# Performance work log

Hardware: AMD Instinct MI355X
Metric: run time of the kernel (lower is better)

## Reference

```python
import jax, jax.numpy as jnp
import numpy as np

N = 4
SEGMENTS = 16
IN_F = 256
OUT_F = 256
BATCH = 512


def chebyshev_lobatto(n):
    # Chebyshev-Lobatto interpolation nodes on [-1, 1]
    k = jnp.arange(n, dtype=jnp.float32)
    return -jnp.cos(jnp.pi * k / (n - 1))


def lagrange_basis(x, nodes):
    # x: [B, In]; returns basis values [B, In, n]
    n = nodes.shape[0]
    cols = []
    for j in range(n):  # n is a small static constant (4)
        terms = [(x - nodes[m]) / (nodes[j] - nodes[m]) for m in range(n) if m != j]
        cols.append(jnp.prod(jnp.stack(terms, axis=0), axis=0))
    return jnp.stack(cols, axis=-1)


def setup_inputs() -> dict:
    key = jax.random.key(0)
    k1, k2 = jax.random.split(key)
    x = jax.random.uniform(k1, (BATCH, IN_F), dtype=jnp.float32, minval=-1.0, maxval=1.0)
    w = jax.random.uniform(
        k2, (OUT_F, IN_F, (N - 1) * SEGMENTS + 1), dtype=jnp.float32, minval=-1.0, maxval=1.0
    )
    return {"x": x, "w": w, "n": N, "segments": SEGMENTS}


def reference(x, w, n, segments):
    nodes = chebyshev_lobatto(n)
    # segment id per element, clamped to [0, segments-1]
    id_min = jnp.clip(((x + 1.0) / 2.0 * segments).astype(jnp.int32), 0, segments - 1)
    id_max = id_min + 1
    wid_min = id_min * (n - 1)  # start of weight slice; slice length == n
    # segment boundaries in x-space: eta(i) = i/segments * 2 - 1
    x_min = id_min.astype(x.dtype) / segments * 2.0 - 1.0
    x_max = id_max.astype(x.dtype) / segments * 2.0 - 1.0
    # rescale x into [-1, 1] within its segment
    x_in = 2.0 * (x - x_min) / (x_max - x_min) - 1.0
    basis = lagrange_basis(x_in, nodes)  # [B, In, n]
    # gather per-element weight slice: w_g[b,i,j,o] = w[o, i, wid_min[b,i]+j]
    idx = wid_min[..., None] + jnp.arange(n)  # [B, In, n]
    w_t = jnp.transpose(w, (1, 2, 0))  # [In, K, Out]
    in_f = w.shape[1]
    w_g = w_t[jnp.arange(in_f)[None, :, None], idx]  # [B, In, n, Out]
    # interpolate and sum over in_features (matches einsum 'ijk,jkli->jl')
    return jnp.einsum("bin,bino->bo", basis, w_g)
```

## Files before the change

kernel.cpp:

```cpp
#include <hip/hip_runtime.h>


typedef _Float16 h2 __attribute__((ext_vector_type(2)));

#define INF     256
#define OUTF    256
#define WSTRIDE 49
#define OSTRIDE (INF * WSTRIDE)
#define PSLICE  (512 * 256)
#define WE_U2   (256 * 16 * 256)
#define BT_U4   (512 * 256)

#define GLOAD16(gptr, lptr)                                                         \
  __builtin_amdgcn_global_load_lds(                                                 \
      (const __attribute__((address_space(1))) unsigned int*)(gptr),                \
      (__attribute__((address_space(3))) unsigned int*)(lptr), 16, 0, 0)

__global__ __launch_bounds__(256)
void pp_prep(const float* __restrict__ x, const float* __restrict__ w,
             uint2* __restrict__ we, uint4* __restrict__ bt) {
    const int blk = blockIdx.x;
    if (blk < 256) {
        const int i = blk, o = threadIdx.x;
        const float* src = w + (size_t)o * OSTRIDE + i * WSTRIDE;
        float t[49];
        #pragma unroll
        for (int k = 0; k < 49; ++k) t[k] = src[k];
        #pragma unroll
        for (int s = 0; s < 16; ++s) {
            auto p0 = __builtin_amdgcn_cvt_pkrtz(t[3*s],   t[3*s+1]);
            auto p1 = __builtin_amdgcn_cvt_pkrtz(t[3*s+2], t[3*s+3]);
            uint2 v;
            v.x = __builtin_bit_cast(unsigned int, p0);
            v.y = __builtin_bit_cast(unsigned int, p1);
            we[((size_t)i * 16 + s) * 256 + o] = v;
        }
    } else {
        const int e = (blk - 256) * 1024 + threadIdx.x * 4;
        float4 xv = *(const float4*)(x + e);
        const float xs[4] = {xv.x, xv.y, xv.z, xv.w};
        #pragma unroll
        for (int q = 0; q < 4; ++q) {
            float xx = xs[q];
            int id = (int)((xx + 1.0f) * 8.0f);
            id = id < 0 ? 0 : (id > 15 ? 15 : id);
            float u = (xx - ((float)id * 0.125f - 1.0f)) * 16.0f - 1.0f;
            float a = u + 1.0f, b2 = u + 0.5f, cc = u - 0.5f, d = u - 1.0f;
            float c0 = b2 * cc * d  * (-2.0f / 3.0f);
            float c1 = a  * cc * d  * ( 4.0f / 3.0f);
            float c2 = a  * b2 * d  * (-4.0f / 3.0f);
            float c3 = a  * b2 * cc * ( 2.0f / 3.0f);
            auto pA = __builtin_amdgcn_cvt_pkrtz(c0, c1);
            auto pB = __builtin_amdgcn_cvt_pkrtz(c2, c3);
            uint4 v;
            v.x = __builtin_bit_cast(unsigned int, pA);
            v.y = __builtin_bit_cast(unsigned int, pB);
            v.z = (unsigned int)id;
            v.w = 0u;
            bt[e + q] = v;
        }
    }
}

__global__ __launch_bounds__(256, 2)
void pp_main(const uint2* __restrict__ we, const uint4* __restrict__ bt,
             float* __restrict__ part) {
    __shared__ uint2 wt[8192];

    const int tid  = threadIdx.x;
    const int wave = __builtin_amdgcn_readfirstlane(tid >> 6);
    const int lane = tid & 63;
    const int i_base = blockIdx.x * 8;
    const int o_base = blockIdx.y * 64;
    const int b0     = blockIdx.z * 128 + wave * 32;

    #pragma unroll
    for (int it = 0; it < 16; ++it) {
        const int u = it * 256 + tid;
        const int i = u >> 9, s = (u >> 5) & 15, g = u & 31;
        const unsigned int* gp = (const unsigned int*)we
            + ((((size_t)(i_base + i) * 16 + s) * 256) + o_base + g * 2) * 2;
        GLOAD16(gp, (unsigned int*)wt + (size_t)u * 4);
    }
    __syncthreads();

    const uint4* btp = bt + ((size_t)b0 * 256 + i_base);
    float* pout = part + (size_t)blockIdx.x * PSLICE + o_base + lane;

    for (int bb = 0; bb < 32; ++bb) {
        const uint4* be = btp + (size_t)bb * 256;
        float acc = 0.0f;
        #pragma unroll
        for (int i = 0; i < 8; ++i) {
            const uint4 B = be[i];
            const h2 cA = __builtin_bit_cast(h2, B.x);
            const h2 cB = __builtin_bit_cast(h2, B.y);
            const uint2 wv = wt[((i * 16 + (int)B.z) << 6) + lane];
            acc = __builtin_amdgcn_fdot2(__builtin_bit_cast(h2, wv.x), cA, acc, false);
            acc = __builtin_amdgcn_fdot2(__builtin_bit_cast(h2, wv.y), cB, acc, false);
        }
        pout[(size_t)(b0 + bb) * 256] = acc;
    }
}

__global__ __launch_bounds__(256)
void pp_reduce(const float* __restrict__ part, float* __restrict__ out) {
    const size_t off4 = (size_t)blockIdx.x * 256 + threadIdx.x;
    const float4* p4 = (const float4*)part;
    float4 s = make_float4(0.f, 0.f, 0.f, 0.f);
    #pragma unroll
    for (int k = 0; k < 32; ++k) {
        float4 v = p4[(size_t)k * (PSLICE / 4) + off4];
        s.x += v.x; s.y += v.y; s.z += v.z; s.w += v.w;
    }
    ((float4*)out)[off4] = s;
}

extern "C" void kernel_launch(void* const* d_in, const int* in_sizes, int n_in,
                              void* d_out, int out_size, void* d_ws, size_t ws_size,
                              hipStream_t stream) {
    const float* x = (const float*)d_in[0];
    const float* w = (const float*)d_in[1];
    float* out = (float*)d_out;
    uint2* we  = (uint2*)d_ws;
    uint4* bt  = (uint4*)((char*)d_ws + (size_t)WE_U2 * 8);
    float* part = (float*)((char*)d_ws + (size_t)WE_U2 * 8
                                       + (size_t)BT_U4 * 16);
    (void)ws_size; (void)n_in; (void)in_sizes; (void)out_size;

    pp_prep<<<dim3(384), 256, 0, stream>>>(x, w, we, bt);
    pp_main<<<dim3(32, 4, 4), 256, 0, stream>>>(we, bt, part);
    pp_reduce<<<dim3(128), 256, 0, stream>>>(part, out);
}
```

Measured before the change: 93.82 us.

## Recast segment-gather interpolation as one-hot dense GEMM on MFMA

The per-segment weight gather is replaced by a dense formulation. Basis coefficients are scattered into a one-hot, segment-expanded A matrix, and weights are laid out as a dense K=64-per-feature B matrix, both written in fp16. A tiled MFMA 16x16x32 GEMM with register-prefetched shared-memory staging computes the split-K partials. This trades a large increase in FLOPs and an extra workspace matrix (~16 MB written and read) for tensor-core throughput in place of scalar fdot2 with LDS gathers.

```diff
diff --git a/kernel.cpp b/kernel.cpp
--- a/kernel.cpp
+++ b/kernel.cpp
@@ -1,106 +1,154 @@
 #include <hip/hip_runtime.h>
 
 
-typedef _Float16 h2 __attribute__((ext_vector_type(2)));
+typedef _Float16 half8 __attribute__((ext_vector_type(8)));
+typedef float f32x4 __attribute__((ext_vector_type(4)));
 
-#define INF     256
-#define OUTF    256
-#define WSTRIDE 49
-#define OSTRIDE (INF * WSTRIDE)
+#define OSTRIDE 12544
 #define PSLICE  (512 * 256)
-#define WE_U2   (256 * 16 * 256)
-#define BT_U4   (512 * 256)
-
-#define GLOAD16(gptr, lptr)                                                         \
-  __builtin_amdgcn_global_load_lds(                                                 \
-      (const __attribute__((address_space(1))) unsigned int*)(gptr),                \
-      (__attribute__((address_space(3))) unsigned int*)(lptr), 16, 0, 0)
+#define WE_U4   (256 * 256 * 8)
+#define AT_U4   (256 * 512 * 8)
 
 __global__ __launch_bounds__(256)
 void pp_prep(const float* __restrict__ x, const float* __restrict__ w,
-             uint2* __restrict__ we, uint4* __restrict__ bt) {
+             uint4* __restrict__ we_t, uint4* __restrict__ A_t) {
+    __shared__ uint4 sm[256 * 9];
+    const int t = threadIdx.x;
     const int blk = blockIdx.x;
+
     if (blk < 256) {
-        const int i = blk, o = threadIdx.x;
-        const float* src = w + (size_t)o * OSTRIDE + i * WSTRIDE;
-        float t[49];
+        const int i = blk;
+        const float* src = w + (size_t)t * OSTRIDE + i * 49;
+        float v[49];
         #pragma unroll
-        for (int k = 0; k < 49; ++k) t[k] = src[k];
+        for (int k = 0; k < 49; ++k) v[k] = src[k];
         #pragma unroll
-        for (int s = 0; s < 16; ++s) {
-            auto p0 = __builtin_amdgcn_cvt_pkrtz(t[3*s],   t[3*s+1]);
-            auto p1 = __builtin_amdgcn_cvt_pkrtz(t[3*s+2], t[3*s+3]);
-            uint2 v;
-            v.x = __builtin_bit_cast(unsigned int, p0);
-            v.y = __builtin_bit_cast(unsigned int, p1);
-            we[((size_t)i * 16 + s) * 256 + o] = v;
+        for (int q = 0; q < 8; ++q) {
+            auto p0 = __builtin_amdgcn_cvt_pkrtz(v[6*q],   v[6*q+1]);
+            auto p1 = __builtin_amdgcn_cvt_pkrtz(v[6*q+2], v[6*q+3]);
+            auto p2 = __builtin_amdgcn_cvt_pkrtz(v[6*q+3], v[6*q+4]);
+            auto p3 = __builtin_amdgcn_cvt_pkrtz(v[6*q+5], v[6*q+6]);
+            uint4 u;
+            u.x = __builtin_bit_cast(unsigned int, p0);
+            u.y = __builtin_bit_cast(unsigned int, p1);
+            u.z = __builtin_bit_cast(unsigned int, p2);
+            u.w = __builtin_bit_cast(unsigned int, p3);
+            sm[t * 9 + q] = u;
+        }
+        __syncthreads();
+        #pragma unroll
+        for (int k = 0; k < 8; ++k) {
+            const int u = k * 256 + t;
+            we_t[(size_t)i * 2048 + u] = sm[(u >> 3) * 9 + (u & 7)];
         }
     } else {
-        const int e = (blk - 256) * 1024 + threadIdx.x * 4;
-        float4 xv = *(const float4*)(x + e);
-        const float xs[4] = {xv.x, xv.y, xv.z, xv.w};
+        const int z = blk - 256;
+        const int i = z >> 1;
+        const int b = (z & 1) * 256 + t;
+        const float xx = x[(size_t)b * 256 + i];
+        int id = (int)((xx + 1.0f) * 8.0f);
+        id = id < 0 ? 0 : (id > 15 ? 15 : id);
+        const float u = (xx - ((float)id * 0.125f - 1.0f)) * 16.0f - 1.0f;
+        const float a = u + 1.0f, b2 = u + 0.5f, cc = u - 0.5f, d = u - 1.0f;
+        const float c0 = b2 * cc * d  * (-2.0f / 3.0f);
+        const float c1 = a  * cc * d  * ( 4.0f / 3.0f);
+        const float c2 = a  * b2 * d  * (-4.0f / 3.0f);
+        const float c3 = a  * b2 * cc * ( 2.0f / 3.0f);
+        auto pA = __builtin_amdgcn_cvt_pkrtz(c0, c1);
+        auto pB = __builtin_amdgcn_cvt_pkrtz(c2, c3);
+        const uint4 z4 = make_uint4(0u, 0u, 0u, 0u);
         #pragma unroll
-        for (int q = 0; q < 4; ++q) {
-            float xx = xs[q];
-            int id = (int)((xx + 1.0f) * 8.0f);
-            id = id < 0 ? 0 : (id > 15 ? 15 : id);
-            float u = (xx - ((float)id * 0.125f - 1.0f)) * 16.0f - 1.0f;
-            float a = u + 1.0f, b2 = u + 0.5f, cc = u - 0.5f, d = u - 1.0f;
-            float c0 = b2 * cc * d  * (-2.0f / 3.0f);
-            float c1 = a  * cc * d  * ( 4.0f / 3.0f);
-            float c2 = a  * b2 * d  * (-4.0f / 3.0f);
-            float c3 = a  * b2 * cc * ( 2.0f / 3.0f);
-            auto pA = __builtin_amdgcn_cvt_pkrtz(c0, c1);
-            auto pB = __builtin_amdgcn_cvt_pkrtz(c2, c3);
-            uint4 v;
-            v.x = __builtin_bit_cast(unsigned int, pA);
-            v.y = __builtin_bit_cast(unsigned int, pB);
-            v.z = (unsigned int)id;
-            v.w = 0u;
-            bt[e + q] = v;
+        for (int q = 0; q < 8; ++q) sm[t * 9 + q] = z4;
+        unsigned int* smu = (unsigned int*)sm;
+        smu[t * 36 + 2 * id]     = __builtin_bit_cast(unsigned int, pA);
+        smu[t * 36 + 2 * id + 1] = __builtin_bit_cast(unsigned int, pB);
+        __syncthreads();
+        uint4* dst = A_t + ((size_t)i * 512 + (z & 1) * 256) * 8;
+        #pragma unroll
+        for (int k = 0; k < 8; ++k) {
+            const int uu = k * 256 + t;
+            dst[uu] = sm[(uu >> 3) * 9 + (uu & 7)];
         }
     }
 }
 
-__global__ __launch_bounds__(256, 2)
-void pp_main(const uint2* __restrict__ we, const uint4* __restrict__ bt,
+__global__ __launch_bounds__(256)
+void pp_gemm(const uint4* __restrict__ A_t, const uint4* __restrict__ we_t,
              float* __restrict__ part) {
-    __shared__ uint2 wt[8192];
+    __shared__ unsigned int smA[128 * 36];
+    __shared__ unsigned int smB[128 * 36];
 
-    const int tid  = threadIdx.x;
-    const int wave = __builtin_amdgcn_readfirstlane(tid >> 6);
-    const int lane = tid & 63;
-    const int i_base = blockIdx.x * 8;
-    const int o_base = blockIdx.y * 64;
-    const int b0     = blockIdx.z * 128 + wave * 32;
+    const int t = threadIdx.x;
+    const int wave = t >> 6, lane = t & 63;
+    const int quad = lane >> 4, l16 = lane & 15;
+    const int ks = blockIdx.x;
+    const int b0 = blockIdx.y * 128;
+    const int o0 = blockIdx.z * 128;
+    const int i_base = ks * 8;
+    const int wm = wave >> 1, wn = wave & 1;
+    const int r = t >> 1, h = t & 1;
+
+    f32x4 acc[4][4];
+    #pragma unroll
+    for (int a = 0; a < 4; ++a)
+        #pragma unroll
+        for (int b = 0; b < 4; ++b) acc[a][b] = (f32x4){0.f, 0.f, 0.f, 0.f};
+
+    uint4 pa[4], pb[4];
+    {
+        const uint4* ga = A_t + ((size_t)i_base * 512 + b0 + r) * 8 + h * 4;
+        const uint4* gb = we_t + ((size_t)i_base * 256 + o0 + r) * 8 + h * 4;
+        #pragma unroll
+        for (int q = 0; q < 4; ++q) { pa[q] = ga[q]; pb[q] = gb[q]; }
+    }
 
     #pragma unroll
-    for (int it = 0; it < 16; ++it) {
-        const int u = it * 256 + tid;
-        const int i = u >> 9, s = (u >> 5) & 15, g = u & 31;
-        const unsigned int* gp = (const unsigned int*)we
-            + ((((size_t)(i_base + i) * 16 + s) * 256) + o_base + g * 2) * 2;
-        GLOAD16(gp, (unsigned int*)wt + (size_t)u * 4);
+    for (int it = 0; it < 8; ++it) {
+        if (it) __syncthreads();
+        #pragma unroll
+        for (int q = 0; q < 4; ++q) {
+            *(uint4*)&smA[r * 36 + h * 16 + q * 4] = pa[q];
+            *(uint4*)&smB[r * 36 + h * 16 + q * 4] = pb[q];
+        }
+        __syncthreads();
+        if (it < 7) {
+            const int i = i_base + it + 1;
+            const uint4* ga = A_t + ((size_t)i * 512 + b0 + r) * 8 + h * 4;
+            const uint4* gb = we_t + ((size_t)i * 256 + o0 + r) * 8 + h * 4;
+            #pragma unroll
+            for (int q = 0; q < 4; ++q) { pa[q] = ga[q]; pb[q] = gb[q]; }
+        }
+        #pragma unroll
+        for (int k2 = 0; k2 < 2; ++k2) {
+            half8 av[4], bv[4];
+            #pragma unroll
+            for (int mi = 0; mi < 4; ++mi)
+                av[mi] = __builtin_bit_cast(half8, *(const uint4*)
+                    &smA[(wm * 64 + mi * 16 + l16) * 36 + k2 * 16 + quad * 4]);
+            #pragma unroll
+            for (int ni = 0; ni < 4; ++ni)
+                bv[ni] = __builtin_bit_cast(half8, *(const uint4*)
+                    &smB[(wn * 64 + ni * 16 + l16) * 36 + k2 * 16 + quad * 4]);
+            #pragma unroll
+            for (int mi = 0; mi < 4; ++mi)
+                #pragma unroll
+                for (int ni = 0; ni < 4; ++ni)
+                    acc[mi][ni] = __builtin_amdgcn_mfma_f32_16x16x32_f16(
+                        av[mi], bv[ni], acc[mi][ni], 0, 0, 0);
+        }
     }
-    __syncthreads();
 
-    const uint4* btp = bt + ((size_t)b0 * 256 + i_base);
-    float* pout = part + (size_t)blockIdx.x * PSLICE + o_base + lane;
-
-    for (int bb = 0; bb < 32; ++bb) {
-        const uint4* be = btp + (size_t)bb * 256;
-        float acc = 0.0f;
+    float* dst = part + (size_t)ks * PSLICE;
+    #pragma unroll
+    for (int mi = 0; mi < 4; ++mi)
         #pragma unroll
-        for (int i = 0; i < 8; ++i) {
-            const uint4 B = be[i];
-            const h2 cA = __builtin_bit_cast(h2, B.x);
-            const h2 cB = __builtin_bit_cast(h2, B.y);
-            const uint2 wv = wt[((i * 16 + (int)B.z) << 6) + lane];
-            acc = __builtin_amdgcn_fdot2(__builtin_bit_cast(h2, wv.x), cA, acc, false);
-            acc = __builtin_amdgcn_fdot2(__builtin_bit_cast(h2, wv.y), cB, acc, false);
+        for (int ni = 0; ni < 4; ++ni) {
+            const int bb = b0 + wm * 64 + mi * 16 + quad * 4;
+            const int oo = o0 + wn * 64 + ni * 16 + l16;
+            #pragma unroll
+            for (int rr = 0; rr < 4; ++rr)
+                dst[(size_t)(bb + rr) * 256 + oo] = acc[mi][ni][rr];
         }
-        pout[(size_t)(b0 + bb) * 256] = acc;
-    }
 }
 
 __global__ __launch_bounds__(256)
@@ -122,13 +170,12 @@
     const float* x = (const float*)d_in[0];
     const float* w = (const float*)d_in[1];
     float* out = (float*)d_out;
-    uint2* we  = (uint2*)d_ws;
-    uint4* bt  = (uint4*)((char*)d_ws + (size_t)WE_U2 * 8);
-    float* part = (float*)((char*)d_ws + (size_t)WE_U2 * 8
-                                       + (size_t)BT_U4 * 16);
+    uint4* we_t = (uint4*)d_ws;
+    uint4* A_t  = we_t + WE_U4;
+    float* part = (float*)(A_t + AT_U4);
     (void)ws_size; (void)n_in; (void)in_sizes; (void)out_size;
 
-    pp_prep<<<dim3(384), 256, 0, stream>>>(x, w, we, bt);
-    pp_main<<<dim3(32, 4, 4), 256, 0, stream>>>(we, bt, part);
+    pp_prep<<<dim3(768), 256, 0, stream>>>(x, w, we_t, A_t);
+    pp_gemm<<<dim3(32, 4, 2), 256, 0, stream>>>(A_t, we_t, part);
     pp_reduce<<<dim3(128), 256, 0, stream>>>(part, out);
 }
```

New measurement: 107.7 us. 1.15x slower.

## Replace LDS-tiled split-K main kernel with direct global gather per output, drop reduce

Applied to the files above, without the earlier changes.

The main kernel no longer stages weight tiles in LDS or splits the input-feature dimension across 32 blocks. Each 64-thread block now owns one batch row and 64 outputs, loops over all 256 inputs, and gathers the fp16 weight pairs straight from global memory. Because each block produces finished outputs, the partial-sum buffer and the separate reduce kernel are removed. The cost is that every weight access becomes an uncached-by-LDS global gather repeated across 512 batch rows, and each thread runs a long serial dependency chain.

```diff
diff --git a/kernel.cpp b/kernel.cpp
--- a/kernel.cpp
+++ b/kernel.cpp
@@ -3,40 +3,31 @@
 
 typedef _Float16 h2 __attribute__((ext_vector_type(2)));
 
-#define INF     256
-#define OUTF    256
-#define WSTRIDE 49
-#define OSTRIDE (INF * WSTRIDE)
-#define PSLICE  (512 * 256)
-#define WE_U2   (256 * 16 * 256)
-#define BT_U4   (512 * 256)
-
-#define GLOAD16(gptr, lptr)                                                         \
-  __builtin_amdgcn_global_load_lds(                                                 \
-      (const __attribute__((address_space(1))) unsigned int*)(gptr),                \
-      (__attribute__((address_space(3))) unsigned int*)(lptr), 16, 0, 0)
+#define OSTRIDE 12544
+#define WP_U2   (256 * 16 * 256)
 
 __global__ __launch_bounds__(256)
 void pp_prep(const float* __restrict__ x, const float* __restrict__ w,
-             uint2* __restrict__ we, uint4* __restrict__ bt) {
+             uint2* __restrict__ wp, uint4* __restrict__ bt) {
+    const int t = threadIdx.x;
     const int blk = blockIdx.x;
     if (blk < 256) {
-        const int i = blk, o = threadIdx.x;
-        const float* src = w + (size_t)o * OSTRIDE + i * WSTRIDE;
-        float t[49];
+        const int i = blk, o = t;
+        const float* src = w + (size_t)o * OSTRIDE + i * 49;
+        float v[49];
         #pragma unroll
-        for (int k = 0; k < 49; ++k) t[k] = src[k];
+        for (int k = 0; k < 49; ++k) v[k] = src[k];
         #pragma unroll
         for (int s = 0; s < 16; ++s) {
-            auto p0 = __builtin_amdgcn_cvt_pkrtz(t[3*s],   t[3*s+1]);
-            auto p1 = __builtin_amdgcn_cvt_pkrtz(t[3*s+2], t[3*s+3]);
-            uint2 v;
-            v.x = __builtin_bit_cast(unsigned int, p0);
-            v.y = __builtin_bit_cast(unsigned int, p1);
-            we[((size_t)i * 16 + s) * 256 + o] = v;
+            auto p0 = __builtin_amdgcn_cvt_pkrtz(v[3*s],   v[3*s+1]);
+            auto p1 = __builtin_amdgcn_cvt_pkrtz(v[3*s+2], v[3*s+3]);
+            uint2 u;
+            u.x = __builtin_bit_cast(unsigned int, p0);
+            u.y = __builtin_bit_cast(unsigned int, p1);
+            wp[((size_t)i * 16 + s) * 256 + o] = u;
         }
     } else {
-        const int e = (blk - 256) * 1024 + threadIdx.x * 4;
+        const int e = (blk - 256) * 1024 + t * 4;
         float4 xv = *(const float4*)(x + e);
         const float xs[4] = {xv.x, xv.y, xv.z, xv.w};
         #pragma unroll
@@ -62,58 +53,25 @@
     }
 }
 
-__global__ __launch_bounds__(256, 2)
-void pp_main(const uint2* __restrict__ we, const uint4* __restrict__ bt,
-             float* __restrict__ part) {
-    __shared__ uint2 wt[8192];
+__global__ __launch_bounds__(64)
+void pp_main(const uint2* __restrict__ wp, const uint4* __restrict__ bt,
+             float* __restrict__ out) {
+    const int lane = threadIdx.x;
+    const int o    = blockIdx.x * 64 + lane;
+    const int b    = blockIdx.y;
+    const uint4* btb = bt + (size_t)b * 256;
 
-    const int tid  = threadIdx.x;
-    const int wave = __builtin_amdgcn_readfirstlane(tid >> 6);
-    const int lane = tid & 63;
-    const int i_base = blockIdx.x * 8;
-    const int o_base = blockIdx.y * 64;
-    const int b0     = blockIdx.z * 128 + wave * 32;
-
-    #pragma unroll
-    for (int it = 0; it < 16; ++it) {
-        const int u = it * 256 + tid;
-        const int i = u >> 9, s = (u >> 5) & 15, g = u & 31;
-        const unsigned int* gp = (const unsigned int*)we
-            + ((((size_t)(i_base + i) * 16 + s) * 256) + o_base + g * 2) * 2;
-        GLOAD16(gp, (unsigned int*)wt + (size_t)u * 4);
+    float acc = 0.0f;
+    #pragma unroll 8
+    for (int i = 0; i < 256; ++i) {
+        const uint4 B = btb[i];
+        const uint2 wv = wp[((size_t)(i * 16 + (int)B.z)) * 256 + o];
+        acc = __builtin_amdgcn_fdot2(__builtin_bit_cast(h2, wv.x),
+                                     __builtin_bit_cast(h2, B.x), acc, false);
+        acc = __builtin_amdgcn_fdot2(__builtin_bit_cast(h2, wv.y),
+                                     __builtin_bit_cast(h2, B.y), acc, false);
     }
-    __syncthreads();
-
-    const uint4* btp = bt + ((size_t)b0 * 256 + i_base);
-    float* pout = part + (size_t)blockIdx.x * PSLICE + o_base + lane;
-
-    for (int bb = 0; bb < 32; ++bb) {
-        const uint4* be = btp + (size_t)bb * 256;
-        float acc = 0.0f;
-        #pragma unroll
-        for (int i = 0; i < 8; ++i) {
-            const uint4 B = be[i];
-            const h2 cA = __builtin_bit_cast(h2, B.x);
-            const h2 cB = __builtin_bit_cast(h2, B.y);
-            const uint2 wv = wt[((i * 16 + (int)B.z) << 6) + lane];
-            acc = __builtin_amdgcn_fdot2(__builtin_bit_cast(h2, wv.x), cA, acc, false);
-            acc = __builtin_amdgcn_fdot2(__builtin_bit_cast(h2, wv.y), cB, acc, false);
-        }
-        pout[(size_t)(b0 + bb) * 256] = acc;
-    }
-}
-
-__global__ __launch_bounds__(256)
-void pp_reduce(const float* __restrict__ part, float* __restrict__ out) {
-    const size_t off4 = (size_t)blockIdx.x * 256 + threadIdx.x;
-    const float4* p4 = (const float4*)part;
-    float4 s = make_float4(0.f, 0.f, 0.f, 0.f);
-    #pragma unroll
-    for (int k = 0; k < 32; ++k) {
-        float4 v = p4[(size_t)k * (PSLICE / 4) + off4];
-        s.x += v.x; s.y += v.y; s.z += v.z; s.w += v.w;
-    }
-    ((float4*)out)[off4] = s;
+    out[(size_t)b * 256 + o] = acc;
 }
 
 extern "C" void kernel_launch(void* const* d_in, const int* in_sizes, int n_in,
@@ -122,13 +80,10 @@
     const float* x = (const float*)d_in[0];
     const float* w = (const float*)d_in[1];
     float* out = (float*)d_out;
-    uint2* we  = (uint2*)d_ws;
-    uint4* bt  = (uint4*)((char*)d_ws + (size_t)WE_U2 * 8);
-    float* part = (float*)((char*)d_ws + (size_t)WE_U2 * 8
-                                       + (size_t)BT_U4 * 16);
+    uint2* wp = (uint2*)d_ws;
+    uint4* bt = (uint4*)((char*)d_ws + (size_t)WP_U2 * 8);
     (void)ws_size; (void)n_in; (void)in_sizes; (void)out_size;
 
-    pp_prep<<<dim3(384), 256, 0, stream>>>(x, w, we, bt);
-    pp_main<<<dim3(32, 4, 4), 256, 0, stream>>>(we, bt, part);
-    pp_reduce<<<dim3(128), 256, 0, stream>>>(part, out);
+    pp_prep<<<dim3(384), 256, 0, stream>>>(x, w, wp, bt);
+    pp_main<<<dim3(4, 512), 64, 0, stream>>>(wp, bt, out);
 }
```

New measurement: 126.4 us. 1.35x slower.
